# Optimization experiments

Measured on AMD Instinct MI355X. Metric: run time of the kernel, lower is better.

## Reference

```python
import jax, jax.numpy as jnp
import numpy as np


def setup_inputs() -> dict:
    key = jax.random.key(0)
    k1, k2, k3, k4, k5 = jax.random.split(key, 5)
    S, B = 512, 256
    E, H, C = 256, 1024, 10
    x = jax.random.randint(k1, (S, B), 0, 10, dtype=jnp.int32)
    emb = jax.random.normal(k2, (10, E), dtype=jnp.float32)
    # orthogonal-ish init is irrelevant for correctness baseline; use scaled normals
    W_hx = jax.random.normal(k3, (E, H), dtype=jnp.float32) / np.sqrt(E)
    W_hh = jax.random.normal(k4, (H, H), dtype=jnp.float32) / np.sqrt(H)
    W_ph = jax.random.normal(k5, (H, C), dtype=jnp.float32) / np.sqrt(H)
    b_h = jnp.zeros((H,), dtype=jnp.float32)
    b_p = jnp.zeros((C,), dtype=jnp.float32)
    return {"x": x, "emb": emb, "W_hx": W_hx, "W_hh": W_hh,
            "W_ph": W_ph, "b_h": b_h, "b_p": b_p}


def reference(x, emb, W_hx, W_hh, W_ph, b_h, b_p):
    S, B = x.shape
    H = W_hh.shape[0]
    # Precompute input projection for all steps in one big GEMM: [S,B,H]
    x_proj = jnp.einsum('sbe,eh->sbh', emb[x], W_hx) + b_h

    def step(state, xp_t):
        state = jnp.tanh(xp_t + state @ W_hh)
        return state, None

    init = jnp.zeros((B, H), dtype=x_proj.dtype)
    state, _ = jax.lax.scan(step, init, x_proj)
    # original detaches the final state before the output projection
    state = jax.lax.stop_gradient(state)
    out = state @ W_ph + b_p  # [B, C]
    return out
```

## Files before the change

### kernel.cpp

```cpp
#include <hip/hip_runtime.h>
#include <hip/hip_bf16.h>


typedef __attribute__((ext_vector_type(8))) short short8;
typedef __attribute__((ext_vector_type(4))) float f32x4;

#define S_LEN 512
#define HDIM  1024
#define NVOC  10

#define OFF_WF    0u
#define OFF_PROJ  2097152u
#define OFF_STBF  2138112u
#define OFF_STF   3186688u
#define OFF_FLAGS 4235264u
#define OFF_XCD   4268032u
#define OFF_SETUP 4269056u

__global__ void zero_flags_k(unsigned int* flags) {
    int id = blockIdx.x * 256 + threadIdx.x;
    if (id < 16 * S_LEN + 256 + 16) flags[id] = 0u;
}

__global__ void proj_k(const float* __restrict__ emb, const float* __restrict__ W_hx,
                       const float* __restrict__ b_h, float* __restrict__ proj) {
    int id = blockIdx.x * 256 + threadIdx.x;
    if (id >= NVOC * HDIM) return;
    int v = id >> 10, h = id & 1023;
    float a = b_h[h];
    #pragma unroll 8
    for (int e = 0; e < 256; ++e) a += emb[v * 256 + e] * W_hx[e * HDIM + h];
    proj[id] = a;
}

static __device__ inline unsigned short f2bf(float f) {
    unsigned u = __builtin_bit_cast(unsigned, f);
    return (unsigned short)((u + 0x7fffu + ((u >> 16) & 1u)) >> 16);
}

__global__ void packw_k(const float* __restrict__ W_hh, unsigned short* __restrict__ Wf) {
    int idx = blockIdx.x * 256 + threadIdx.x;
    int lane = idx & 63, kk = (idx >> 6) & 31, nt = idx >> 11;
    int k0 = kk * 32 + (lane >> 4) * 8;
    int col = nt * 16 + (lane & 15);
    short8 v;
    #pragma unroll
    for (int j = 0; j < 8; ++j) v[j] = (short)f2bf(W_hh[(k0 + j) * HDIM + col]);
    *(short8*)(Wf + (size_t)idx * 8) = v;
}

__global__ __launch_bounds__(256, 1) void rnn_steps_k(
    const int* __restrict__ x, const unsigned short* __restrict__ Wf,
    const float* __restrict__ proj, unsigned short* __restrict__ stbf,
    float* __restrict__ stf, unsigned int* __restrict__ flags,
    unsigned int* __restrict__ xcdmap, unsigned int* __restrict__ setupf)
{
    const int bid = blockIdx.x;
    const int g   = ((bid & 7) << 1) | ((bid >> 3) & 1);
    const int wgn = bid >> 4;
    const int tid = threadIdx.x;
    const int wave = tid >> 6, lane = tid & 63;
    const int b0 = g << 4;
    const int nt = (wgn << 2) + wave;
    const int n0 = nt << 4;
    const int wg_n0 = wgn << 6;
    const int row = lane & 15;
    const int kl  = lane >> 4;

    __shared__ __align__(16) char Abuf[32768];
    __shared__ unsigned char xl[S_LEN * 16];
    __shared__ float pl[NVOC * 64];
    __shared__ unsigned uni_sh;

    unsigned xcd;
    asm("s_getreg_b32 %0, hwreg(HW_REG_XCC_ID)" : "=s"(xcd));
    if (tid == 0) {
        xcdmap[(g << 4) + wgn] = xcd;
        __hip_atomic_fetch_add(setupf + g, 1u, __ATOMIC_RELEASE, __HIP_MEMORY_SCOPE_AGENT);
        while (__hip_atomic_load(setupf + g, __ATOMIC_ACQUIRE, __HIP_MEMORY_SCOPE_AGENT) < 16u) {}
        unsigned u = 1u;
        for (int i = 0; i < 16; ++i) {
            unsigned v = __hip_atomic_load(xcdmap + (g << 4) + i,
                                           __ATOMIC_RELAXED, __HIP_MEMORY_SCOPE_AGENT);
            u &= (unsigned)(v == xcd);
        }
        uni_sh = u;
    }

    for (int i = tid; i < S_LEN * 16; i += 256)
        xl[i] = (unsigned char)x[((i >> 4) << 8) + b0 + (i & 15)];
    for (int i = tid; i < NVOC * 64; i += 256)
        pl[i] = proj[(i >> 6) * HDIM + wg_n0 + (i & 63)];

    short8 bfr[32];
    const short8* wp = (const short8*)Wf;
    #pragma unroll
    for (int kk = 0; kk < 32; ++kk)
        bfr[kk] = wp[((nt << 5) + kk) * 64 + lane];

    __syncthreads();
    const bool uniform = (uni_sh != 0u);

    const int sw = (row & 7) << 4;
    const int abase = row << 11;
    const int klb = kl << 4;

    for (int s = 0; s < S_LEN; ++s) {
        f32x4 acc0 = {0.f, 0.f, 0.f, 0.f};
        f32x4 acc1 = acc0, acc2 = acc0, acc3 = acc0;
        if (s > 0) {
            if (tid == 0) {
                const unsigned int* fp = flags + (g << 9) + (s - 1);
                while (__hip_atomic_load(fp, __ATOMIC_RELAXED, __HIP_MEMORY_SCOPE_AGENT) < 16u) {}
            }
            __syncthreads();
            const char* src = (const char*)stbf + (((s - 1) & 1) << 19) + (g << 15);
            if (uniform) {
                #pragma unroll
                for (int it = 0; it < 8; ++it) {
                    int o = (it * 256 + tid) * 16;
                    int arow = o >> 11;
                    int soff = (arow << 11) + ((o & 2047) ^ ((arow & 7) << 4));
                    __builtin_amdgcn_global_load_lds(
                        (const __attribute__((address_space(1))) void*)(src + soff),
                        (__attribute__((address_space(3))) void*)(Abuf + it * 4096 + wave * 1024),
                        16, 0, 1);
                }
            } else {
                #pragma unroll
                for (int it = 0; it < 8; ++it) {
                    int o = (it * 256 + tid) * 16;
                    int arow = o >> 11;
                    int soff = (arow << 11) + ((o & 2047) ^ ((arow & 7) << 4));
                    __builtin_amdgcn_global_load_lds(
                        (const __attribute__((address_space(1))) void*)(src + soff),
                        (__attribute__((address_space(3))) void*)(Abuf + it * 4096 + wave * 1024),
                        16, 0, 17);
                }
            }
            __syncthreads();
            #pragma unroll
            for (int kk = 0; kk < 32; kk += 4) {
                short8 a0 = *(const short8*)(Abuf + abase + ((((kk + 0) << 6) + klb) ^ sw));
                short8 a1 = *(const short8*)(Abuf + abase + ((((kk + 1) << 6) + klb) ^ sw));
                short8 a2 = *(const short8*)(Abuf + abase + ((((kk + 2) << 6) + klb) ^ sw));
                short8 a3 = *(const short8*)(Abuf + abase + ((((kk + 3) << 6) + klb) ^ sw));
                acc0 = __builtin_amdgcn_mfma_f32_16x16x32_bf16(a0, bfr[kk + 0], acc0, 0, 0, 0);
                acc1 = __builtin_amdgcn_mfma_f32_16x16x32_bf16(a1, bfr[kk + 1], acc1, 0, 0, 0);
                acc2 = __builtin_amdgcn_mfma_f32_16x16x32_bf16(a2, bfr[kk + 2], acc2, 0, 0, 0);
                acc3 = __builtin_amdgcn_mfma_f32_16x16x32_bf16(a3, bfr[kk + 3], acc3, 0, 0, 0);
            }
        }
        f32x4 accs = acc0 + acc1 + acc2 + acc3;
        #pragma unroll
        for (int j = 0; j < 4; ++j) {
            int r = (kl << 2) + j;
            int xv = xl[(s << 4) + r];
            float p = pl[(xv << 6) + (wave << 4) + row];
            float z = accs[j] + p;
            z = fminf(15.f, fmaxf(-15.f, z));
            float e = exp2f(z * 2.885390082f);
            float th = (e - 1.f) / (e + 1.f);
            if (s < S_LEN - 1) {
                stbf[((s & 1) << 18) + ((b0 + r) << 10) + n0 + row] = f2bf(th);
            } else {
                stf[((b0 + r) << 10) + n0 + row] = th;
            }
        }
        if (s < S_LEN - 1) {
            __syncthreads();
            if (tid == 0) {
                if (uniform) {
                    __hip_atomic_fetch_add(flags + (g << 9) + s, 1u,
                                           __ATOMIC_RELAXED, __HIP_MEMORY_SCOPE_AGENT);
                } else {
                    __hip_atomic_fetch_add(flags + (g << 9) + s, 1u,
                                           __ATOMIC_RELEASE, __HIP_MEMORY_SCOPE_AGENT);
                }
            }
        }
    }
}

__global__ void outproj_k(const float* __restrict__ stf, const float* __restrict__ W_ph,
                          const float* __restrict__ b_p, float* __restrict__ out) {
    int b = blockIdx.x, t = threadIdx.x;
    float acc[10];
    #pragma unroll
    for (int c = 0; c < 10; ++c) acc[c] = 0.f;
    for (int h = t; h < HDIM; h += 256) {
        float sv = stf[b * HDIM + h];
        const float* w = W_ph + h * 10;
        #pragma unroll
        for (int c = 0; c < 10; ++c) acc[c] += sv * w[c];
    }
    __shared__ float red[256][10];
    #pragma unroll
    for (int c = 0; c < 10; ++c) red[t][c] = acc[c];
    __syncthreads();
    for (int off = 128; off > 0; off >>= 1) {
        if (t < off) {
            #pragma unroll
            for (int c = 0; c < 10; ++c) red[t][c] += red[t + off][c];
        }
        __syncthreads();
    }
    if (t < 10) out[b * 10 + t] = red[0][t] + b_p[t];
}

extern "C" void kernel_launch(void* const* d_in, const int* in_sizes, int n_in,
                              void* d_out, int out_size, void* d_ws, size_t ws_size,
                              hipStream_t stream) {
    const int*   x    = (const int*)d_in[0];
    const float* emb  = (const float*)d_in[1];
    const float* W_hx = (const float*)d_in[2];
    const float* W_hh = (const float*)d_in[3];
    const float* W_ph = (const float*)d_in[4];
    const float* b_h  = (const float*)d_in[5];
    const float* b_p  = (const float*)d_in[6];

    char* ws = (char*)d_ws;
    unsigned short* Wf     = (unsigned short*)(ws + OFF_WF);
    float*          proj   = (float*)(ws + OFF_PROJ);
    unsigned short* stbf   = (unsigned short*)(ws + OFF_STBF);
    float*          stf    = (float*)(ws + OFF_STF);
    unsigned int*   flags  = (unsigned int*)(ws + OFF_FLAGS);
    unsigned int*   xcdmap = (unsigned int*)(ws + OFF_XCD);
    unsigned int*   setupf = (unsigned int*)(ws + OFF_SETUP);

    zero_flags_k<<<34, 256, 0, stream>>>(flags);
    proj_k<<<40, 256, 0, stream>>>(emb, W_hx, b_h, proj);
    packw_k<<<512, 256, 0, stream>>>(W_hh, Wf);
    rnn_steps_k<<<256, 256, 0, stream>>>(x, Wf, proj, stbf, stf, flags, xcdmap, setupf);
    outproj_k<<<256, 256, 0, stream>>>(stf, W_ph, b_p, (float*)d_out);
}
```

Before: 1.138 ms.

## Replace per-step counter barrier with per-wave flags, wave-parallel polling and double-buffered LDS

Each wave now publishes its progress through its own padded flag (storing the step number) instead of atomically incrementing one shared counter per step. Every wave polls all 64 flags of its group in parallel across lanes, which removes a workgroup barrier before the poll and another before the flag publish. The LDS A-buffer is double-buffered so the next step's loads cannot overwrite data still being read. The projection table is also padded in LDS. This targets the inter-workgroup synchronization latency on the 512-step serial critical path, at the cost of more polling traffic and more LDS use.

```diff
diff --git a/kernel.cpp b/kernel.cpp
--- a/kernel.cpp
+++ b/kernel.cpp
@@ -14,12 +14,12 @@
 #define OFF_STBF  2138112u
 #define OFF_STF   3186688u
 #define OFF_FLAGS 4235264u
-#define OFF_XCD   4268032u
-#define OFF_SETUP 4269056u
+#define OFF_XCD   4300800u
+#define OFF_SETUP 4301824u
 
 __global__ void zero_flags_k(unsigned int* flags) {
     int id = blockIdx.x * 256 + threadIdx.x;
-    if (id < 16 * S_LEN + 256 + 16) flags[id] = 0u;
+    if (id < 16384 + 256 + 16) flags[id] = 0u;
 }
 
 __global__ void proj_k(const float* __restrict__ emb, const float* __restrict__ W_hx,
@@ -67,9 +67,9 @@
     const int row = lane & 15;
     const int kl  = lane >> 4;
 
-    __shared__ __align__(16) char Abuf[32768];
+    __shared__ __align__(16) char Abuf[2][32768];
     __shared__ unsigned char xl[S_LEN * 16];
-    __shared__ float pl[NVOC * 64];
+    __shared__ float pl[NVOC * 68];
     __shared__ unsigned uni_sh;
 
     unsigned xcd;
@@ -89,8 +89,11 @@
 
     for (int i = tid; i < S_LEN * 16; i += 256)
         xl[i] = (unsigned char)x[((i >> 4) << 8) + b0 + (i & 15)];
-    for (int i = tid; i < NVOC * 64; i += 256)
-        pl[i] = proj[(i >> 6) * HDIM + wg_n0 + (i & 63)];
+    if (tid < 64) {
+        #pragma unroll
+        for (int v = 0; v < NVOC; ++v)
+            pl[v * 68 + tid] = proj[v * HDIM + wg_n0 + tid];
+    }
 
     short8 bfr[32];
     const short8* wp = (const short8*)Wf;
@@ -104,16 +107,18 @@
     const int sw = (row & 7) << 4;
     const int abase = row << 11;
     const int klb = kl << 4;
+    unsigned int* myflag  = flags + (g << 10) + (((wgn << 2) + wave) << 4);
+    const unsigned int* pollp = flags + (g << 10) + (lane << 4);
 
     for (int s = 0; s < S_LEN; ++s) {
         f32x4 acc0 = {0.f, 0.f, 0.f, 0.f};
         f32x4 acc1 = acc0, acc2 = acc0, acc3 = acc0;
         if (s > 0) {
-            if (tid == 0) {
-                const unsigned int* fp = flags + (g << 9) + (s - 1);
-                while (__hip_atomic_load(fp, __ATOMIC_RELAXED, __HIP_MEMORY_SCOPE_AGENT) < 16u) {}
-            }
-            __syncthreads();
+            unsigned v;
+            do {
+                v = __hip_atomic_load(pollp, __ATOMIC_RELAXED, __HIP_MEMORY_SCOPE_AGENT);
+            } while (__any((int)(v < (unsigned)s)));
+            char* dst = Abuf[s & 1];
             const char* src = (const char*)stbf + (((s - 1) & 1) << 19) + (g << 15);
             if (uniform) {
                 #pragma unroll
@@ -123,7 +128,7 @@
                     int soff = (arow << 11) + ((o & 2047) ^ ((arow & 7) << 4));
                     __builtin_amdgcn_global_load_lds(
                         (const __attribute__((address_space(1))) void*)(src + soff),
-                        (__attribute__((address_space(3))) void*)(Abuf + it * 4096 + wave * 1024),
+                        (__attribute__((address_space(3))) void*)(dst + it * 4096 + wave * 1024),
                         16, 0, 1);
                 }
             } else {
@@ -134,17 +139,20 @@
                     int soff = (arow << 11) + ((o & 2047) ^ ((arow & 7) << 4));
                     __builtin_amdgcn_global_load_lds(
                         (const __attribute__((address_space(1))) void*)(src + soff),
-                        (__attribute__((address_space(3))) void*)(Abuf + it * 4096 + wave * 1024),
+                        (__attribute__((address_space(3))) void*)(dst + it * 4096 + wave * 1024),
                         16, 0, 17);
                 }
             }
-            __syncthreads();
+            asm volatile("s_waitcnt vmcnt(0)" ::: "memory");
+            __builtin_amdgcn_s_barrier();
+            __builtin_amdgcn_sched_barrier(0);
+            const char* ab = dst + abase;
             #pragma unroll
             for (int kk = 0; kk < 32; kk += 4) {
-                short8 a0 = *(const short8*)(Abuf + abase + ((((kk + 0) << 6) + klb) ^ sw));
-                short8 a1 = *(const short8*)(Abuf + abase + ((((kk + 1) << 6) + klb) ^ sw));
-                short8 a2 = *(const short8*)(Abuf + abase + ((((kk + 2) << 6) + klb) ^ sw));
-                short8 a3 = *(const short8*)(Abuf + abase + ((((kk + 3) << 6) + klb) ^ sw));
+                short8 a0 = *(const short8*)(ab + ((((kk + 0) << 6) + klb) ^ sw));
+                short8 a1 = *(const short8*)(ab + ((((kk + 1) << 6) + klb) ^ sw));
+                short8 a2 = *(const short8*)(ab + ((((kk + 2) << 6) + klb) ^ sw));
+                short8 a3 = *(const short8*)(ab + ((((kk + 3) << 6) + klb) ^ sw));
                 acc0 = __builtin_amdgcn_mfma_f32_16x16x32_bf16(a0, bfr[kk + 0], acc0, 0, 0, 0);
                 acc1 = __builtin_amdgcn_mfma_f32_16x16x32_bf16(a1, bfr[kk + 1], acc1, 0, 0, 0);
                 acc2 = __builtin_amdgcn_mfma_f32_16x16x32_bf16(a2, bfr[kk + 2], acc2, 0, 0, 0);
@@ -156,7 +164,7 @@
         for (int j = 0; j < 4; ++j) {
             int r = (kl << 2) + j;
             int xv = xl[(s << 4) + r];
-            float p = pl[(xv << 6) + (wave << 4) + row];
+            float p = pl[xv * 68 + (wave << 4) + row];
             float z = accs[j] + p;
             z = fminf(15.f, fmaxf(-15.f, z));
             float e = exp2f(z * 2.885390082f);
@@ -168,14 +176,14 @@
             }
         }
         if (s < S_LEN - 1) {
-            __syncthreads();
-            if (tid == 0) {
+            asm volatile("s_waitcnt vmcnt(0)" ::: "memory");
+            if (lane == 0) {
                 if (uniform) {
-                    __hip_atomic_fetch_add(flags + (g << 9) + s, 1u,
-                                           __ATOMIC_RELAXED, __HIP_MEMORY_SCOPE_AGENT);
+                    __hip_atomic_store(myflag, (unsigned)(s + 1),
+                                       __ATOMIC_RELAXED, __HIP_MEMORY_SCOPE_AGENT);
                 } else {
-                    __hip_atomic_fetch_add(flags + (g << 9) + s, 1u,
-                                           __ATOMIC_RELEASE, __HIP_MEMORY_SCOPE_AGENT);
+                    __hip_atomic_store(myflag, (unsigned)(s + 1),
+                                       __ATOMIC_RELEASE, __HIP_MEMORY_SCOPE_AGENT);
                 }
             }
         }
@@ -228,7 +236,7 @@
     unsigned int*   xcdmap = (unsigned int*)(ws + OFF_XCD);
     unsigned int*   setupf = (unsigned int*)(ws + OFF_SETUP);
 
-    zero_flags_k<<<34, 256, 0, stream>>>(flags);
+    zero_flags_k<<<66, 256, 0, stream>>>(flags);
     proj_k<<<40, 256, 0, stream>>>(emb, W_hx, b_h, proj);
     packw_k<<<512, 256, 0, stream>>>(W_hh, Wf);
     rnn_steps_k<<<256, 256, 0, stream>>>(x, Wf, proj, stbf, stf, flags, xcdmap, setupf);
```

New measurement: 1.535 ms. 34.9% more time.
